# Performance work log

Hardware: AMD Instinct MI355X
Metric: run time of the kernel (lower is better)

Reference implementation:

```python
import jax, jax.numpy as jnp
import numpy as np

N_HEAD = 16
MASK_VALUE = -10000.0


def setup_inputs() -> dict:
    key = jax.random.key(0)
    ks = jax.random.split(key, 5)
    B, S, D = 2, 2048, 1024
    return {
        "x": jax.random.normal(ks[0], (B, S, D), dtype=jnp.float32),
        "qkv_w": jax.random.normal(ks[1], (D, 3 * D), dtype=jnp.float32) * 0.02,
        "qkv_b": jnp.zeros((3 * D,), dtype=jnp.float32),
        "proj_w": jax.random.normal(ks[2], (D, D), dtype=jnp.float32) * 0.02,
        "proj_b": jnp.zeros((D,), dtype=jnp.float32),
    }


def reference(x, qkv_w, qkv_b, proj_w, proj_b):
    B, S, D = x.shape
    H = N_HEAD
    hd = D // H

    # fused QKV projection, then split (torch.split along last dim)
    qkv = x @ qkv_w + qkv_b                      # [B, S, 3D]
    q, k, v = jnp.split(qkv, 3, axis=-1)

    def split_heads(t):  # [B, S, D] -> [B, H, S, hd]
        return t.reshape(B, S, H, hd).transpose(0, 2, 1, 3)

    q, k, v = split_heads(q), split_heads(k), split_heads(v)

    # scaled dot-product scores (scale_attn_weights=True)
    scores = jnp.einsum("bhqd,bhkd->bhqk", q, k) / jnp.sqrt(jnp.asarray(hd, x.dtype))

    # causal mask: tril over [query_len, key_len] (no cache, so q_len == k_len == S)
    causal = jnp.tril(jnp.ones((S, S), dtype=bool))[None, None]
    scores = jnp.where(causal, scores, jnp.asarray(MASK_VALUE, x.dtype))

    attn = jax.nn.softmax(scores, axis=-1)       # dropout p=0 (eval): identity
    out = jnp.einsum("bhqk,bhkd->bhqd", attn, v)

    # merge heads and output projection (resid dropout p=0)
    out = out.transpose(0, 2, 1, 3).reshape(B, S, D)
    out = out @ proj_w + proj_b
    return out
```

## Files before the change

kernel.cpp:

```cpp
#include <hip/hip_runtime.h>
#include <hip/hip_bf16.h>


#define SEQ 2048
#define DM 1024
#define HD 64
#define NHEAD 16
#define BHTOT 32

typedef unsigned short u16;
typedef __bf16 bf16_t;
typedef bf16_t bf16x8 __attribute__((ext_vector_type(8)));
typedef float f32x4 __attribute__((ext_vector_type(4)));
typedef float f32x16 __attribute__((ext_vector_type(16)));

__device__ __forceinline__ u16 f2bf(float f) {
  unsigned u = __float_as_uint(f);
  u += 0x7fffu + ((u >> 16) & 1u);
  return (u16)(u >> 16);
}

__device__ __forceinline__ f32x4 mfma16(uint4 a, uint4 b, f32x4 c) {
  return __builtin_amdgcn_mfma_f32_16x16x32_bf16(
      __builtin_bit_cast(bf16x8, a), __builtin_bit_cast(bf16x8, b), c, 0, 0, 0);
}

__device__ __forceinline__ f32x16 mfma32(uint4 a, uint4 b, f32x16 c) {
  return __builtin_amdgcn_mfma_f32_32x32x16_bf16(
      __builtin_bit_cast(bf16x8, a), __builtin_bit_cast(bf16x8, b), c, 0, 0, 0);
}

__device__ __forceinline__ unsigned cvtpk(float lo, float hi) {
  unsigned d;
  asm("v_cvt_pk_bf16_f32 %0, %1, %2" : "=v"(d) : "v"(lo), "v"(hi));
  return d;
}

__device__ __forceinline__ void gload_lds16(const u16* g, void* l) {
  __builtin_amdgcn_global_load_lds(
      (const __attribute__((address_space(1))) unsigned*)g,
      (__attribute__((address_space(3))) unsigned*)l, 16, 0, 0);
}

__device__ __forceinline__ void ttile(const float* __restrict__ W,
                                      u16* __restrict__ Wt, int K, int N,
                                      int n0, int k0) {
  __shared__ u16 t[32][132];
  const int tid = threadIdx.x;
  const int tx = tid & 31, ty = tid >> 5;
#pragma unroll
  for (int i = 0; i < 4; ++i) {
    const int k = ty + i * 8;
    float4 v = *(const float4*)(W + (size_t)(k0 + k) * N + n0 + tx * 4);
    t[k][tx * 4 + 0] = f2bf(v.x);
    t[k][tx * 4 + 1] = f2bf(v.y);
    t[k][tx * 4 + 2] = f2bf(v.z);
    t[k][tx * 4 + 3] = f2bf(v.w);
  }
  __syncthreads();
  const int n = tid >> 1, half = tid & 1;
  u16 tmp[16];
#pragma unroll
  for (int j = 0; j < 16; ++j) tmp[j] = t[half * 16 + j][n];
  uint4 lo, hi;
  lo.x = (unsigned)tmp[0] | ((unsigned)tmp[1] << 16);
  lo.y = (unsigned)tmp[2] | ((unsigned)tmp[3] << 16);
  lo.z = (unsigned)tmp[4] | ((unsigned)tmp[5] << 16);
  lo.w = (unsigned)tmp[6] | ((unsigned)tmp[7] << 16);
  hi.x = (unsigned)tmp[8] | ((unsigned)tmp[9] << 16);
  hi.y = (unsigned)tmp[10] | ((unsigned)tmp[11] << 16);
  hi.z = (unsigned)tmp[12] | ((unsigned)tmp[13] << 16);
  hi.w = (unsigned)tmp[14] | ((unsigned)tmp[15] << 16);
  u16* base = Wt + (size_t)(n0 + n) * K + k0 + half * 16;
  *(uint4*)base = lo;
  *(uint4*)(base + 8) = hi;
}

__global__ __launch_bounds__(256) void prep(
    const float* __restrict__ x, const float* __restrict__ wqkv,
    const float* __restrict__ wproj, u16* __restrict__ xb,
    u16* __restrict__ wqkvT, u16* __restrict__ wprojT) {
  const int bid = blockIdx.x;
  if (bid < 4096) {
    int i = (bid * 256 + threadIdx.x) * 4;
    float4 v = *(const float4*)(x + i);
    uint2 pk;
    pk.x = (unsigned)f2bf(v.x) | ((unsigned)f2bf(v.y) << 16);
    pk.y = (unsigned)f2bf(v.z) | ((unsigned)f2bf(v.w) << 16);
    *(uint2*)(xb + i) = pk;
  } else if (bid < 4096 + 768) {
    const int tb = bid - 4096;
    const int nt = tb % 24, kt = tb / 24;
    ttile(wqkv, wqkvT, DM, 3072, nt * 128, kt * 32);
  } else {
    const int tb = bid - 4864;
    const int nt = tb & 7, kt = tb >> 3;
    ttile(wproj, wprojT, DM, DM, nt * 128, kt * 32);
  }
}

__global__ __launch_bounds__(256) void qkv_gemm(
    const u16* __restrict__ A, const u16* __restrict__ Bt,
    const float* __restrict__ bias,
    u16* __restrict__ qb, u16* __restrict__ kb, u16* __restrict__ vb) {
  __shared__ u16 Al[128 * 32];
  __shared__ u16 Bl[128 * 32];
  const int tid = threadIdx.x;
  const int m0 = blockIdx.y * 128;
  const int n0 = blockIdx.x * 128;
  const int w = tid >> 6, lane = tid & 63;
  const int lr = lane & 15, lg = lane >> 4;
  const int wm = (w >> 1) * 64, wn = (w & 1) * 64;
  const int Kd = DM;

  f32x4 acc[4][4] = {};

  for (int kk = 0; kk < Kd; kk += 32) {
    __syncthreads();
#pragma unroll
    for (int i = 0; i < 2; ++i) {
      int off = (i * 4 + w) * 1024 + lane * 16;
      int row = off >> 6, colb = off & 63;
      gload_lds16(A + (size_t)(m0 + row) * Kd + kk + (colb >> 1),
                  (char*)Al + (i * 4 + w) * 1024);
      gload_lds16(Bt + (size_t)(n0 + row) * Kd + kk + (colb >> 1),
                  (char*)Bl + (i * 4 + w) * 1024);
    }
    __syncthreads();
    uint4 af[4], bfr[4];
#pragma unroll
    for (int mi = 0; mi < 4; ++mi)
      af[mi] = *(const uint4*)(Al + (wm + mi * 16 + lr) * 32 + lg * 8);
#pragma unroll
    for (int ni = 0; ni < 4; ++ni)
      bfr[ni] = *(const uint4*)(Bl + (wn + ni * 16 + lr) * 32 + lg * 8);
#pragma unroll
    for (int mi = 0; mi < 4; ++mi)
#pragma unroll
      for (int ni = 0; ni < 4; ++ni)
        acc[mi][ni] = mfma16(af[mi], bfr[ni], acc[mi][ni]);
  }

#pragma unroll
  for (int mi = 0; mi < 4; ++mi) {
#pragma unroll
    for (int ni = 0; ni < 4; ++ni) {
#pragma unroll
      for (int r = 0; r < 4; ++r) {
        int m = m0 + wm + mi * 16 + lg * 4 + r;
        int n = n0 + wn + ni * 16 + lr;
        float v = acc[mi][ni][r] + bias[n];
        int part = n >> 10;
        int d = n & 1023;
        int h = d >> 6, dim = d & 63;
        int b = m >> 11, s = m & 2047;
        int bh = b * NHEAD + h;
        if (part == 0)
          qb[((size_t)bh * SEQ + s) * HD + dim] = f2bf(v * 0.18033688f);
        else if (part == 1)
          kb[((size_t)bh * SEQ + s) * HD + dim] = f2bf(v);
        else
          vb[((size_t)bh * HD + dim) * SEQ + s] = f2bf(v);
      }
    }
  }
}

__global__ __launch_bounds__(128) void attn_kernel(
    const u16* __restrict__ Q, const u16* __restrict__ K,
    const u16* __restrict__ Vt, u16* __restrict__ O) {
  const int lane = threadIdx.x & 63;
  const int w = threadIdx.x >> 6;
  const int r31 = lane & 31;
  const int hi = lane >> 5;
  const int bh = blockIdx.x & 31;
  const int j = 31 - (blockIdx.x >> 5);
  const int qt = 2 * j + w;
  const int q0w = qt * 32;
  const int nst = j + 1;

  const u16* Qb = Q + (size_t)bh * SEQ * HD;
  const u16* Kb = K + (size_t)bh * SEQ * HD;
  const u16* Vb = Vt + (size_t)bh * HD * SEQ;

  uint4 qf[4];
#pragma unroll
  for (int ks = 0; ks < 4; ++ks)
    qf[ks] = *(const uint4*)(Qb + (size_t)(q0w + r31) * HD + ks * 16 + hi * 8);

  f32x16 ot0 = {}, ot1 = {};
  float L = 0.f;

#define LOADK(KF, kv0)                                                          \
  {                                                                             \
    _Pragma("unroll") for (int ks = 0; ks < 4; ++ks) {                          \
      KF[ks] = *(const uint4*)(Kb + (size_t)((kv0) + r31) * HD + ks * 16 + hi * 8); \
      KF[ks + 4] =                                                              \
          *(const uint4*)(Kb + (size_t)((kv0) + 32 + r31) * HD + ks * 16 + hi * 8); \
    }                                                                           \
  }

#define RELAYOUT(dst, S, base)                                                  \
  {                                                                             \
    unsigned e01 = cvtpk(S[base + 0], S[base + 1]), e23 = cvtpk(S[base + 2], S[base + 3]); \
    unsigned e45 = cvtpk(S[base + 4], S[base + 5]), e67 = cvtpk(S[base + 6], S[base + 7]); \
    unsigned p01 = __shfl_xor(e01, 32), p23 = __shfl_xor(e23, 32);              \
    unsigned p45 = __shfl_xor(e45, 32), p67 = __shfl_xor(e67, 32);              \
    dst.x = hi ? p45 : e01;                                                     \
    dst.y = hi ? p67 : e23;                                                     \
    dst.z = hi ? e45 : p01;                                                     \
    dst.w = hi ? e67 : p23;                                                     \
  }

#define STEP(KF, KN)                                                            \
  {                                                                             \
    const int kv0 = t << 6;                                                     \
    const bool last = (t == nst - 1);                                           \
    const bool skip1 = last && ((qt & 1) == 0);   \
    uint4 vf[8];                                                                \
    _Pragma("unroll") for (int ks = 0; ks < 2; ++ks) {                          \
      vf[ks] = *(const uint4*)(Vb + (size_t)r31 * SEQ + kv0 + ks * 16 + hi * 8); \
      vf[ks + 4] =                                                              \
          *(const uint4*)(Vb + (size_t)(32 + r31) * SEQ + kv0 + ks * 16 + hi * 8); \
    }                                                                           \
    if (!skip1) {                                                               \
      _Pragma("unroll") for (int ks = 2; ks < 4; ++ks) {                        \
        vf[ks] = *(const uint4*)(Vb + (size_t)r31 * SEQ + kv0 + ks * 16 + hi * 8); \
        vf[ks + 4] =                                                            \
            *(const uint4*)(Vb + (size_t)(32 + r31) * SEQ + kv0 + ks * 16 + hi * 8); \
      }                                                                         \
    }                                                                           \
    f32x16 s0 = {}, s1 = {};                                                    \
    _Pragma("unroll") for (int ks = 0; ks < 4; ++ks)                            \
        s0 = mfma32(KF[ks], qf[ks], s0);                                        \
    if (!skip1) {                                                               \
      _Pragma("unroll") for (int ks = 0; ks < 4; ++ks)                          \
          s1 = mfma32(KF[ks + 4], qf[ks], s1);                                  \
    }                                                                           \
    if (t + 1 < nst) LOADK(KN, kv0 + 64);                                       \
    if (last) {                                                                 \
      _Pragma("unroll") for (int i = 0; i < 16; ++i) {                          \
        const int row = (i & 3) + 8 * (i >> 2) + 4 * hi;                        \
        if (skip1) {                                                            \
          if (row > r31) s0[i] = -1e30f;                                        \
        } else {                                                                \
          if (row > r31) s1[i] = -1e30f;                                        \
        }                                                                       \
      }                                                                         \
    }                                                                           \
    float rs = 0.f;                                                             \
    _Pragma("unroll") for (int i = 0; i < 16; ++i) {                            \
      s0[i] = __builtin_exp2f(s0[i]);                                           \
      rs += s0[i];                                                              \
    }                                                                           \
    if (!skip1) {                                                               \
      _Pragma("unroll") for (int i = 0; i < 16; ++i) {                          \
        s1[i] = __builtin_exp2f(s1[i]);                                         \
        rs += s1[i];                                                            \
      }                                                                         \
    }                                                                           \
    L += rs;                                                                    \
    uint4 pa[4];                                                                \
    RELAYOUT(pa[0], s0, 0);                                                     \
    RELAYOUT(pa[1], s0, 8);                                                     \
    if (!skip1) {                                                               \
      RELAYOUT(pa[2], s1, 0);                                                   \
      RELAYOUT(pa[3], s1, 8);                                                   \
    }                                                                           \
    _Pragma("unroll") for (int ks = 0; ks < 2; ++ks) {                          \
      ot0 = mfma32(vf[ks], pa[ks], ot0);                                        \
      ot1 = mfma32(vf[ks + 4], pa[ks], ot1);                                    \
    }                                                                           \
    if (!skip1) {                                                               \
      _Pragma("unroll") for (int ks = 2; ks < 4; ++ks) {                        \
        ot0 = mfma32(vf[ks], pa[ks], ot0);                                      \
        ot1 = mfma32(vf[ks + 4], pa[ks], ot1);                                  \
      }                                                                         \
    }                                                                           \
  }

  uint4 kA[8], kB[8];
  LOADK(kA, 0);
  int t = 0;
  for (;;) {
    STEP(kA, kB);
    if (++t >= nst) break;
    STEP(kB, kA);
    if (++t >= nst) break;
  }
#undef STEP
#undef RELAYOUT
#undef LOADK

  L += __shfl_xor(L, 32);
  const float inv = 1.0f / L;
  const int b = bh >> 4, h = bh & 15;
  u16* Orow = O + ((size_t)b * SEQ + q0w + r31) * DM + h * HD;
#pragma unroll
  for (int g = 0; g < 4; ++g) {
    uint2 p0, p1;
    p0.x = (unsigned)f2bf(ot0[4 * g + 0] * inv) | ((unsigned)f2bf(ot0[4 * g + 1] * inv) << 16);
    p0.y = (unsigned)f2bf(ot0[4 * g + 2] * inv) | ((unsigned)f2bf(ot0[4 * g + 3] * inv) << 16);
    p1.x = (unsigned)f2bf(ot1[4 * g + 0] * inv) | ((unsigned)f2bf(ot1[4 * g + 1] * inv) << 16);
    p1.y = (unsigned)f2bf(ot1[4 * g + 2] * inv) | ((unsigned)f2bf(ot1[4 * g + 3] * inv) << 16);
    *(uint2*)(Orow + 8 * g + 4 * hi) = p0;
    *(uint2*)(Orow + 32 + 8 * g + 4 * hi) = p1;
  }
}

__global__ __launch_bounds__(256) void proj_gemm(
    const u16* __restrict__ A, const u16* __restrict__ Bt,
    const float* __restrict__ bias, float* __restrict__ out) {
  __shared__ u16 Al[128 * 32];
  __shared__ u16 Bl[64 * 32];
  const int tid = threadIdx.x;
  const int m0 = blockIdx.y * 128;
  const int n0 = blockIdx.x * 64;
  const int w = tid >> 6, lane = tid & 63;
  const int lr = lane & 15, lg = lane >> 4;
  const int wm = w * 32;
  const int Kd = DM;

  f32x4 acc[2][4] = {};

  for (int kk = 0; kk < Kd; kk += 32) {
    __syncthreads();
#pragma unroll
    for (int i = 0; i < 2; ++i) {
      int off = (i * 4 + w) * 1024 + lane * 16;
      int row = off >> 6, colb = off & 63;
      gload_lds16(A + (size_t)(m0 + row) * Kd + kk + (colb >> 1),
                  (char*)Al + (i * 4 + w) * 1024);
    }
    {
      int off = w * 1024 + lane * 16;
      int row = off >> 6, colb = off & 63;
      gload_lds16(Bt + (size_t)(n0 + row) * Kd + kk + (colb >> 1),
                  (char*)Bl + w * 1024);
    }
    __syncthreads();
    uint4 af[2], bfr[4];
#pragma unroll
    for (int mi = 0; mi < 2; ++mi)
      af[mi] = *(const uint4*)(Al + (wm + mi * 16 + lr) * 32 + lg * 8);
#pragma unroll
    for (int ni = 0; ni < 4; ++ni)
      bfr[ni] = *(const uint4*)(Bl + (ni * 16 + lr) * 32 + lg * 8);
#pragma unroll
    for (int mi = 0; mi < 2; ++mi)
#pragma unroll
      for (int ni = 0; ni < 4; ++ni)
        acc[mi][ni] = mfma16(af[mi], bfr[ni], acc[mi][ni]);
  }

#pragma unroll
  for (int mi = 0; mi < 2; ++mi)
#pragma unroll
    for (int ni = 0; ni < 4; ++ni)
#pragma unroll
      for (int r = 0; r < 4; ++r) {
        int m = m0 + wm + mi * 16 + lg * 4 + r;
        int n = n0 + ni * 16 + lr;
        out[(size_t)m * DM + n] = acc[mi][ni][r] + bias[n];
      }
}

extern "C" void kernel_launch(void* const* d_in, const int* in_sizes, int n_in,
                              void* d_out, int out_size, void* d_ws, size_t ws_size,
                              hipStream_t stream) {
  const float* x      = (const float*)d_in[0];
  const float* qkv_w  = (const float*)d_in[1];
  const float* qkv_b  = (const float*)d_in[2];
  const float* proj_w = (const float*)d_in[3];
  const float* proj_b = (const float*)d_in[4];
  float* out = (float*)d_out;

  const size_t per = (size_t)BHTOT * SEQ * HD;
  u16* qb = (u16*)d_ws;
  u16* kb = qb + per;
  u16* vb = kb + per;
  u16* xb = vb + per;
  u16* ab = xb;
  u16* wqkvT = xb + (size_t)SEQ * 2 * DM;
  u16* wprojT = wqkvT + (size_t)3072 * DM;

  dim3 blk(256);
  prep<<<dim3(5120), blk, 0, stream>>>(x, qkv_w, proj_w, xb, wqkvT, wprojT);
  qkv_gemm<<<dim3(24, 32), blk, 0, stream>>>(xb, wqkvT, qkv_b, qb, kb, vb);
  attn_kernel<<<dim3(1024), dim3(128), 0, stream>>>(qb, kb, vb, ab);
  proj_gemm<<<dim3(16, 32), blk, 0, stream>>>(ab, wprojT, proj_b, out);
}
```

Before: 140.7 us.

## Double GEMM K-tile to 64 with XOR-swizzled LDS layout and packed V stores

The QKV and output-projection GEMMs now stage 64-wide K slices per iteration instead of 32, halving the number of barrier pairs per K loop. The global-to-LDS loads place chunks using an XOR swizzle, and fragment reads apply the matching swizzle to avoid LDS bank conflicts. The QKV epilogue hoists bias and index math per fragment and writes the transposed V output as one packed 8-byte store per fragment. LDS use per block doubles, which may reduce occupancy.

```diff
diff --git a/kernel.cpp b/kernel.cpp
--- a/kernel.cpp
+++ b/kernel.cpp
@@ -103,8 +103,8 @@
     const u16* __restrict__ A, const u16* __restrict__ Bt,
     const float* __restrict__ bias,
     u16* __restrict__ qb, u16* __restrict__ kb, u16* __restrict__ vb) {
-  __shared__ u16 Al[128 * 32];
-  __shared__ u16 Bl[128 * 32];
+  __shared__ u16 Al[128 * 64];
+  __shared__ u16 Bl[128 * 64];
   const int tid = threadIdx.x;
   const int m0 = blockIdx.y * 128;
   const int n0 = blockIdx.x * 128;
@@ -112,55 +112,67 @@
   const int lr = lane & 15, lg = lane >> 4;
   const int wm = (w >> 1) * 64, wn = (w & 1) * 64;
   const int Kd = DM;
+  const int srow = lane >> 3;
+  const int scol = ((lane & 7) ^ srow) << 3;
 
   f32x4 acc[4][4] = {};
 
-  for (int kk = 0; kk < Kd; kk += 32) {
+  for (int kk = 0; kk < Kd; kk += 64) {
     __syncthreads();
 #pragma unroll
-    for (int i = 0; i < 2; ++i) {
-      int off = (i * 4 + w) * 1024 + lane * 16;
-      int row = off >> 6, colb = off & 63;
-      gload_lds16(A + (size_t)(m0 + row) * Kd + kk + (colb >> 1),
-                  (char*)Al + (i * 4 + w) * 1024);
-      gload_lds16(Bt + (size_t)(n0 + row) * Kd + kk + (colb >> 1),
-                  (char*)Bl + (i * 4 + w) * 1024);
+    for (int i = 0; i < 4; ++i) {
+      const int c = i * 4 + w;
+      const int row = c * 8 + srow;
+      gload_lds16(A + (size_t)(m0 + row) * Kd + kk + scol, (char*)Al + c * 1024);
+      gload_lds16(Bt + (size_t)(n0 + row) * Kd + kk + scol, (char*)Bl + c * 1024);
     }
     __syncthreads();
-    uint4 af[4], bfr[4];
-#pragma unroll
-    for (int mi = 0; mi < 4; ++mi)
-      af[mi] = *(const uint4*)(Al + (wm + mi * 16 + lr) * 32 + lg * 8);
-#pragma unroll
-    for (int ni = 0; ni < 4; ++ni)
-      bfr[ni] = *(const uint4*)(Bl + (wn + ni * 16 + lr) * 32 + lg * 8);
-#pragma unroll
-    for (int mi = 0; mi < 4; ++mi)
+#pragma unroll
+    for (int h2 = 0; h2 < 2; ++h2) {
+      const int sl = (((h2 * 4 + lg) ^ (lr & 7)) << 3);
+      uint4 af[4], bfr[4];
+#pragma unroll
+      for (int mi = 0; mi < 4; ++mi)
+        af[mi] = *(const uint4*)(Al + (wm + mi * 16 + lr) * 64 + sl);
 #pragma unroll
       for (int ni = 0; ni < 4; ++ni)
-        acc[mi][ni] = mfma16(af[mi], bfr[ni], acc[mi][ni]);
+        bfr[ni] = *(const uint4*)(Bl + (wn + ni * 16 + lr) * 64 + sl);
+#pragma unroll
+      for (int mi = 0; mi < 4; ++mi)
+#pragma unroll
+        for (int ni = 0; ni < 4; ++ni)
+          acc[mi][ni] = mfma16(af[mi], bfr[ni], acc[mi][ni]);
+    }
   }
 
 #pragma unroll
   for (int mi = 0; mi < 4; ++mi) {
 #pragma unroll
     for (int ni = 0; ni < 4; ++ni) {
-#pragma unroll
-      for (int r = 0; r < 4; ++r) {
-        int m = m0 + wm + mi * 16 + lg * 4 + r;
-        int n = n0 + wn + ni * 16 + lr;
-        float v = acc[mi][ni][r] + bias[n];
-        int part = n >> 10;
-        int d = n & 1023;
-        int h = d >> 6, dim = d & 63;
-        int b = m >> 11, s = m & 2047;
-        int bh = b * NHEAD + h;
-        if (part == 0)
-          qb[((size_t)bh * SEQ + s) * HD + dim] = f2bf(v * 0.18033688f);
-        else if (part == 1)
-          kb[((size_t)bh * SEQ + s) * HD + dim] = f2bf(v);
-        else
-          vb[((size_t)bh * HD + dim) * SEQ + s] = f2bf(v);
+      const int n = n0 + wn + ni * 16 + lr;
+      const float bv = bias[n];
+      const int part = n >> 10;
+      const int d = n & 1023;
+      const int h = d >> 6, dim = d & 63;
+      const int m_base = m0 + wm + mi * 16 + lg * 4;
+      const int b = m_base >> 11, s = m_base & 2047;
+      const int bh = b * NHEAD + h;
+      if (part == 0) {
+        u16* p = qb + ((size_t)bh * SEQ + s) * HD + dim;
+#pragma unroll
+        for (int r = 0; r < 4; ++r)
+          p[r * HD] = f2bf((acc[mi][ni][r] + bv) * 0.18033688f);
+      } else if (part == 1) {
+        u16* p = kb + ((size_t)bh * SEQ + s) * HD + dim;
+#pragma unroll
+        for (int r = 0; r < 4; ++r) p[r * HD] = f2bf(acc[mi][ni][r] + bv);
+      } else {
+        uint2 pk;
+        pk.x = (unsigned)f2bf(acc[mi][ni][0] + bv) |
+               ((unsigned)f2bf(acc[mi][ni][1] + bv) << 16);
+        pk.y = (unsigned)f2bf(acc[mi][ni][2] + bv) |
+               ((unsigned)f2bf(acc[mi][ni][3] + bv) << 16);
+        *(uint2*)(vb + ((size_t)bh * HD + dim) * SEQ + s) = pk;
       }
     }
   }
@@ -311,8 +323,8 @@
 __global__ __launch_bounds__(256) void proj_gemm(
     const u16* __restrict__ A, const u16* __restrict__ Bt,
     const float* __restrict__ bias, float* __restrict__ out) {
-  __shared__ u16 Al[128 * 32];
-  __shared__ u16 Bl[64 * 32];
+  __shared__ u16 Al[128 * 64];
+  __shared__ u16 Bl[64 * 64];
   const int tid = threadIdx.x;
   const int m0 = blockIdx.y * 128;
   const int n0 = blockIdx.x * 64;
@@ -320,37 +332,42 @@
   const int lr = lane & 15, lg = lane >> 4;
   const int wm = w * 32;
   const int Kd = DM;
+  const int srow = lane >> 3;
+  const int scol = ((lane & 7) ^ srow) << 3;
 
   f32x4 acc[2][4] = {};
 
-  for (int kk = 0; kk < Kd; kk += 32) {
+  for (int kk = 0; kk < Kd; kk += 64) {
     __syncthreads();
 #pragma unroll
+    for (int i = 0; i < 4; ++i) {
+      const int c = i * 4 + w;
+      const int row = c * 8 + srow;
+      gload_lds16(A + (size_t)(m0 + row) * Kd + kk + scol, (char*)Al + c * 1024);
+    }
+#pragma unroll
     for (int i = 0; i < 2; ++i) {
-      int off = (i * 4 + w) * 1024 + lane * 16;
-      int row = off >> 6, colb = off & 63;
-      gload_lds16(A + (size_t)(m0 + row) * Kd + kk + (colb >> 1),
-                  (char*)Al + (i * 4 + w) * 1024);
-    }
-    {
-      int off = w * 1024 + lane * 16;
-      int row = off >> 6, colb = off & 63;
-      gload_lds16(Bt + (size_t)(n0 + row) * Kd + kk + (colb >> 1),
-                  (char*)Bl + w * 1024);
+      const int c = i * 4 + w;
+      const int row = c * 8 + srow;
+      gload_lds16(Bt + (size_t)(n0 + row) * Kd + kk + scol, (char*)Bl + c * 1024);
     }
     __syncthreads();
-    uint4 af[2], bfr[4];
-#pragma unroll
-    for (int mi = 0; mi < 2; ++mi)
-      af[mi] = *(const uint4*)(Al + (wm + mi * 16 + lr) * 32 + lg * 8);
-#pragma unroll
-    for (int ni = 0; ni < 4; ++ni)
-      bfr[ni] = *(const uint4*)(Bl + (ni * 16 + lr) * 32 + lg * 8);
-#pragma unroll
-    for (int mi = 0; mi < 2; ++mi)
+#pragma unroll
+    for (int h2 = 0; h2 < 2; ++h2) {
+      const int sl = (((h2 * 4 + lg) ^ (lr & 7)) << 3);
+      uint4 af[2], bfr[4];
+#pragma unroll
+      for (int mi = 0; mi < 2; ++mi)
+        af[mi] = *(const uint4*)(Al + (wm + mi * 16 + lr) * 64 + sl);
 #pragma unroll
       for (int ni = 0; ni < 4; ++ni)
-        acc[mi][ni] = mfma16(af[mi], bfr[ni], acc[mi][ni]);
+        bfr[ni] = *(const uint4*)(Bl + (ni * 16 + lr) * 64 + sl);
+#pragma unroll
+      for (int mi = 0; mi < 2; ++mi)
+#pragma unroll
+        for (int ni = 0; ni < 4; ++ni)
+          acc[mi][ni] = mfma16(af[mi], bfr[ni], acc[mi][ni]);
+    }
   }
 
 #pragma unroll
```

Result: no change. 140.3 us (-0.3%).
